# Kernel tuning notes

Hardware: AMD Instinct MI355X
Metric: run time of the kernel (lower is better)

Reference implementation:

```python
import jax, jax.numpy as jnp
import numpy as np

B, L, D = 2, 2048, 1024
N_HEADS, N_KV_HEADS = 16, 4
HEAD_DIM = D // N_HEADS
WINDOW = 1024
ROPE_BASE = 10000.0


def setup_inputs() -> dict:
    key = jax.random.key(0)
    ks = jax.random.split(key, 5)
    s = 0.02
    return {
        "x": jax.random.normal(ks[0], (B, L, D), jnp.float32),
        "Wq": jax.random.normal(ks[1], (D, N_HEADS * HEAD_DIM), jnp.float32) * s,
        "Wk": jax.random.normal(ks[2], (D, N_KV_HEADS * HEAD_DIM), jnp.float32) * s,
        "Wv": jax.random.normal(ks[3], (D, N_KV_HEADS * HEAD_DIM), jnp.float32) * s,
        "Wo": jax.random.normal(ks[4], (N_HEADS * HEAD_DIM, D), jnp.float32) * s,
    }


def _rope_cos_sin(seq_len, head_dim, dtype):
    inv_freq = 1.0 / (ROPE_BASE ** (jnp.arange(0, head_dim, 2, dtype=jnp.float32) / head_dim))
    angles = jnp.arange(seq_len, dtype=jnp.float32)[:, None] * inv_freq[None, :]  # [L, d/2]
    emb = jnp.concatenate([angles, angles], axis=-1)  # [L, d]
    return jnp.cos(emb).astype(dtype), jnp.sin(emb).astype(dtype)


def _rotate_half(t):
    t1, t2 = jnp.split(t, 2, axis=-1)
    return jnp.concatenate([-t2, t1], axis=-1)


def reference(x, Wq, Wk, Wv, Wo):
    b, l, d = x.shape
    q = (x @ Wq).reshape(b, l, N_HEADS, HEAD_DIM).transpose(0, 2, 1, 3)      # [B,H,L,d]
    k = (x @ Wk).reshape(b, l, N_KV_HEADS, HEAD_DIM).transpose(0, 2, 1, 3)   # [B,Kv,L,d]
    v = (x @ Wv).reshape(b, l, N_KV_HEADS, HEAD_DIM).transpose(0, 2, 1, 3)

    cos, sin = _rope_cos_sin(l, HEAD_DIM, x.dtype)  # [L,d]
    q = q * cos[None, None] + _rotate_half(q) * sin[None, None]
    k = k * cos[None, None] + _rotate_half(k) * sin[None, None]

    # GQA: expand kv heads to query heads
    group = N_HEADS // N_KV_HEADS
    k = jnp.repeat(k, group, axis=1)  # [B,H,L,d]
    v = jnp.repeat(v, group, axis=1)

    scale = 1.0 / np.sqrt(HEAD_DIM)
    scores = jnp.einsum("bhqd,bhkd->bhqk", q, k) * scale  # [B,H,L,L]

    # sliding-window causal mask: attend to j with j <= i and i - j < WINDOW
    i = jnp.arange(l)[:, None]
    j = jnp.arange(l)[None, :]
    allowed = (j <= i) & (i - j < WINDOW)
    scores = jnp.where(allowed[None, None], scores, jnp.finfo(scores.dtype).min)

    attn = jax.nn.softmax(scores, axis=-1)
    out = jnp.einsum("bhqk,bhkd->bhqd", attn, v)           # [B,H,L,d]
    out = out.transpose(0, 2, 1, 3).reshape(b, l, N_HEADS * HEAD_DIM)
    return out @ Wo  # [B,L,D]; dropout p=0 is identity
```

## Files before the change

kernel.cpp:

```cpp
#include <hip/hip_runtime.h>

typedef unsigned short u16;
typedef unsigned int u32;
typedef short short8 __attribute__((ext_vector_type(8)));
typedef float f32x4 __attribute__((ext_vector_type(4)));

#define N_B 2
#define N_L 2048
#define N_D 1024
#define N_H 16
#define N_KVH 4
#define HDIM 64
#define WINDOW 1024

#define QSCALE (0.125f * 1.44269504088896f)

__device__ __forceinline__ u16 f2bf(float f) {
  unsigned u = __builtin_bit_cast(unsigned, f);
  u = u + 0x7fffu + ((u >> 16) & 1u);
  return (u16)(u >> 16);
}

__device__ __forceinline__ u32 pk2bf(float lo, float hi) {
  u32 a = __builtin_bit_cast(u32, lo) + 0x8000u;
  u32 b = __builtin_bit_cast(u32, hi) + 0x8000u;
  return __builtin_amdgcn_perm(b, a, 0x07060302u);
}

__device__ __forceinline__ void gl2lds16(const u16* g, u16* l) {
  __builtin_amdgcn_global_load_lds((const __attribute__((address_space(1))) void*)g,
                                   (__attribute__((address_space(3))) void*)l, 16, 0, 0);
}


__global__ __launch_bounds__(256) void prep_kernel(
    const float* __restrict__ x, const float* __restrict__ Wq, const float* __restrict__ Wk,
    const float* __restrict__ Wv, const float* __restrict__ Wo,
    u16* __restrict__ xb, u16* __restrict__ wqkvT, u16* __restrict__ woT,
    float* __restrict__ rc, float* __restrict__ rs) {
  __shared__ float tbuf[32][33];
  int bid = blockIdx.x, tid = threadIdx.x;
  if (bid < 1024) {
    size_t base = ((size_t)bid * 256 + tid) * 16;
    u32 o[8];
#pragma unroll
    for (int j = 0; j < 4; j++) {
      float4 f = *(const float4*)&x[base + j * 4];
      o[2 * j] = pk2bf(f.x, f.y);
      o[2 * j + 1] = pk2bf(f.z, f.w);
    }
    *(uint4*)&xb[base] = *(uint4*)&o[0];
    *(uint4*)&xb[base + 8] = *(uint4*)&o[4];
  } else if (bid < 3584) {
    const float* src;
    u16* dst;
    int gx, t, shift;
    if (bid < 2048) { src = Wq; dst = wqkvT; gx = 32; shift = 5; t = bid - 1024; }
    else if (bid < 2304) { src = Wk; dst = wqkvT + 1024 * 1024; gx = 8; shift = 3; t = bid - 2048; }
    else if (bid < 2560) { src = Wv; dst = wqkvT + 1280 * 1024; gx = 8; shift = 3; t = bid - 2304; }
    else { src = Wo; dst = woT; gx = 32; shift = 5; t = bid - 2560; }
    int srcN = gx * 32;
    int n0 = (t & (gx - 1)) * 32, k0 = (t >> shift) * 32;
    int lx = tid & 31, ly = tid >> 5;
#pragma unroll
    for (int q = 0; q < 4; q++)
      tbuf[ly + 8 * q][lx] = src[(k0 + ly + 8 * q) * srcN + n0 + lx];
    __syncthreads();
#pragma unroll
    for (int q = 0; q < 4; q++)
      dst[(n0 + ly + 8 * q) * 1024 + k0 + lx] = f2bf(tbuf[lx][ly + 8 * q]);
  } else {
    int idx = (bid - 3584) * 256 + tid;
    int i = idx >> 5, j = idx & 31;
    float inv = powf(10000.0f, -(float)j * (1.0f / 32.0f));
    float ang = (float)i * inv;
    rc[idx] = cosf(ang);
    rs[idx] = sinf(ang);
  }
}


template <int MODE>
__global__ __launch_bounds__(256, 2) void gemm_kernel(
    const u16* __restrict__ A, const u16* __restrict__ Bt,
    u16* __restrict__ qo, u16* __restrict__ ko, u16* __restrict__ vo,
    float* __restrict__ fo, const float* __restrict__ rc, const float* __restrict__ rs) {
  __shared__ u16 smem[65536 / 2];
  int tid = threadIdx.x;
  int w = tid >> 6, lane = tid & 63, quad = lane >> 4, r = lane & 15;
  int rx = r & 7;
  int wm = w >> 1, wn = w & 1;
  int m0 = blockIdx.y * 128, n0 = blockIdx.x * 128;

  f32x4 acc[4][4];
#pragma unroll
  for (int a_ = 0; a_ < 4; a_++)
#pragma unroll
    for (int b_ = 0; b_ < 4; b_++) acc[a_][b_] = {0.f, 0.f, 0.f, 0.f};

  auto stage = [&](int kt, int buf) {
    u16* a_s = smem + buf * 8192;
    u16* b_s = smem + 16384 + buf * 8192;
#pragma unroll
    for (int it = 0; it < 4; ++it) {
      int cc = it * 256 + tid;
      int row = cc >> 3, p = cc & 7, c = p ^ (row & 7);
      gl2lds16(&A[(size_t)(m0 + row) * 1024 + kt * 64 + c * 8], &a_s[cc * 8]);
    }
#pragma unroll
    for (int it = 0; it < 4; ++it) {
      int cc = it * 256 + tid;
      int row = cc >> 3, p = cc & 7, c = p ^ (row & 7);
      gl2lds16(&Bt[(size_t)(n0 + row) * 1024 + kt * 64 + c * 8], &b_s[cc * 8]);
    }
  };

  stage(0, 0);
  for (int kt = 0; kt < 16; ++kt) {
    int buf = kt & 1;
    __syncthreads();
    if (kt + 1 < 16) stage(kt + 1, buf ^ 1);
    u16* a_s = smem + buf * 8192;
    u16* b_s = smem + 16384 + buf * 8192;
#pragma unroll
    for (int ks = 0; ks < 2; ks++) {
      int pc = (ks * 4 + quad) ^ rx;
      short8 af[4], bfr[4];
#pragma unroll
      for (int tm = 0; tm < 4; tm++)
        af[tm] = *(const short8*)&a_s[(wm * 64 + tm * 16 + r) * 64 + pc * 8];
#pragma unroll
      for (int tn = 0; tn < 4; tn++)
        bfr[tn] = *(const short8*)&b_s[(wn * 64 + tn * 16 + r) * 64 + pc * 8];
#pragma unroll
      for (int tm = 0; tm < 4; tm++)
#pragma unroll
        for (int tn = 0; tn < 4; tn++)
          acc[tm][tn] = __builtin_amdgcn_mfma_f32_16x16x32_bf16(af[tm], bfr[tn], acc[tm][tn], 0, 0, 0);
    }
  }

  int nbase = n0 + wn * 64;
  if constexpr (MODE == 0) {
    if (nbase < 1024) {
      int h = nbase >> 6;
#pragma unroll
      for (int tm = 0; tm < 4; tm++) {
#pragma unroll
        for (int reg = 0; reg < 4; reg++) {
          int m = m0 + wm * 64 + tm * 16 + quad * 4 + reg;
          int b = m >> 11, i = m & 2047;
          size_t base = ((size_t)(b * N_H + h) * N_L + i) * HDIM;
#pragma unroll
          for (int tn = 0; tn < 2; tn++) {
            int dlo = tn * 16 + r;
            float c = rc[i * 32 + dlo], s = rs[i * 32 + dlo];
            float vlo = acc[tm][tn][reg], vhi = acc[tm][tn + 2][reg];
            qo[base + dlo] = f2bf((vlo * c - vhi * s) * QSCALE);
            qo[base + dlo + 32] = f2bf((vhi * c + vlo * s) * QSCALE);
          }
        }
      }
    } else if (nbase < 1280) {
      int h = (nbase - 1024) >> 6;
#pragma unroll
      for (int tm = 0; tm < 4; tm++) {
#pragma unroll
        for (int reg = 0; reg < 4; reg++) {
          int m = m0 + wm * 64 + tm * 16 + quad * 4 + reg;
          int b = m >> 11, i = m & 2047;
          size_t base = ((size_t)(b * N_KVH + h) * N_L + i) * HDIM;
#pragma unroll
          for (int tn = 0; tn < 2; tn++) {
            int dlo = tn * 16 + r;
            float c = rc[i * 32 + dlo], s = rs[i * 32 + dlo];
            float vlo = acc[tm][tn][reg], vhi = acc[tm][tn + 2][reg];
            ko[base + dlo] = f2bf(vlo * c - vhi * s);
            ko[base + dlo + 32] = f2bf(vhi * c + vlo * s);
          }
        }
      }
    } else {
      __syncthreads();
      int hkv = (nbase - 1280) >> 6;
      int bb = (m0 + wm * 64) >> 11;
      int tbase = (m0 + wm * 64) & 2047;
      u16* myvs = smem + w * 4608;
#pragma unroll
      for (int tm = 0; tm < 4; tm++) {
#pragma unroll
        for (int tn = 0; tn < 4; tn++) {
          uint2 pk;
          pk.x = pk2bf(acc[tm][tn][0], acc[tm][tn][1]);
          pk.y = pk2bf(acc[tm][tn][2], acc[tm][tn][3]);
          *(uint2*)&myvs[(tn * 16 + r) * 72 + tm * 16 + quad * 4] = pk;
        }
      }
      __asm__ volatile("s_waitcnt lgkmcnt(0)" ::: "memory");
      u16* vtb = vo + (size_t)((bb * N_KVH + hkv) * 64) * 2048;
#pragma unroll
      for (int q2 = 0; q2 < 8; ++q2) {
        int flat = q2 * 64 + lane;
        int row = flat >> 3, part = flat & 7;
        uint4 val = *(uint4*)&myvs[row * 72 + part * 8];
        *(uint4*)&vtb[row * 2048 + tbase + part * 8] = val;
      }
    }
  } else {
#pragma unroll
    for (int tm = 0; tm < 4; tm++) {
#pragma unroll
      for (int reg = 0; reg < 4; reg++) {
        int m = m0 + wm * 64 + tm * 16 + quad * 4 + reg;
#pragma unroll
        for (int tn = 0; tn < 4; tn++)
          fo[(size_t)m * 1024 + nbase + tn * 16 + r] = acc[tm][tn][reg];
      }
    }
  }
}


__global__ __launch_bounds__(256) void attn_kernel(
    const u16* __restrict__ Q, const u16* __restrict__ K,
    const u16* __restrict__ Vt, u16* __restrict__ O) {
  __shared__ u16 k_s[2][64 * 64];
  __shared__ u16 v_s[2][64 * 64];
  __shared__ u16 pt[4][16 * 64];
  int tid = threadIdx.x, w = tid >> 6, lane = tid & 63, quad = lane >> 4, r = lane & 15;
  int qb = 31 - blockIdx.x;
  int h = blockIdx.y, b = blockIdx.z;
  int i0 = qb * 64;
  int hk = h >> 2;
  int qw0 = i0 + w * 16;
  int iq = qw0 + r;

  const u16* qptr = Q + (size_t)((b * N_H + h) * N_L + iq) * HDIM;
  short8 qf[2];
  qf[0] = *(const short8*)&qptr[quad * 8];
  qf[1] = *(const short8*)&qptr[32 + quad * 8];

  const u16* kbase = K + (size_t)(b * N_KVH + hk) * N_L * HDIM;
  const u16* vtbase = Vt + (size_t)(b * N_KVH + hk) * HDIM * N_L;

  auto stage = [&](int jt, int buf) {
#pragma unroll
    for (int it = 0; it < 2; ++it) {
      int cc = it * 256 + tid;
      int row = cc >> 3, p = cc & 7, c = p ^ (row & 7);
      gl2lds16(&kbase[(size_t)(jt * 64 + row) * 64 + c * 8], &k_s[buf][cc * 8]);
    }
#pragma unroll
    for (int it = 0; it < 2; ++it) {
      int cc = it * 256 + tid;
      int row = cc >> 3, p = cc & 7, c = p ^ (row & 7);
      gl2lds16(&vtbase[(size_t)row * 2048 + jt * 64 + c * 8], &v_s[buf][cc * 8]);
    }
  };

  float l_lane = 0.f;
  f32x4 o_acc[4];
#pragma unroll
  for (int tm = 0; tm < 4; tm++) o_acc[tm] = {0.f, 0.f, 0.f, 0.f};

  int jt0 = (i0 >= WINDOW) ? ((i0 - (WINDOW - 1)) >> 6) : 0;
  int nt = qb - jt0 + 1;
  u16* mypt = pt[w];
  int rx = r & 7;

  stage(jt0, 0);

  for (int t = 0; t < nt; ++t) {
    int jt = jt0 + t, j0 = jt << 6, buf = t & 1;
    __syncthreads();
    if (t + 1 < nt) stage(jt + 1, buf ^ 1);

    f32x4 s_acc[4];
#pragma unroll
    for (int tm = 0; tm < 4; tm++) s_acc[tm] = {0.f, 0.f, 0.f, 0.f};
#pragma unroll
    for (int ks = 0; ks < 2; ks++) {
      int pc = (ks * 4 + quad) ^ rx;
#pragma unroll
      for (int tm = 0; tm < 4; tm++) {
        short8 kf = *(const short8*)&k_s[buf][(tm * 16 + r) * 64 + pc * 8];
        s_acc[tm] = __builtin_amdgcn_mfma_f32_16x16x32_bf16(kf, qf[ks], s_acc[tm], 0, 0, 0);
      }
    }

    bool interior = (j0 + 63 <= qw0) && (qw0 + 15 - j0 < WINDOW);
    if (!interior) {
#pragma unroll
      for (int tm = 0; tm < 4; tm++) {
#pragma unroll
        for (int reg = 0; reg < 4; reg++) {
          int j = j0 + tm * 16 + quad * 4 + reg;
          bool ok = (j <= iq) && (iq - j < WINDOW);
          if (!ok) s_acc[tm][reg] = -1e30f;
        }
      }
    }

    float p[4][4];
#pragma unroll
    for (int tm = 0; tm < 4; tm++)
#pragma unroll
      for (int reg = 0; reg < 4; reg++) {
        float e = __builtin_amdgcn_exp2f(s_acc[tm][reg]);
        p[tm][reg] = e;
        l_lane += e;
      }

#pragma unroll
    for (int tm = 0; tm < 4; tm++) {
      uint2 pk;
      pk.x = pk2bf(p[tm][0], p[tm][1]);
      pk.y = pk2bf(p[tm][2], p[tm][3]);
      int c = tm * 2 + (quad >> 1), half = quad & 1;
      int pp = c ^ rx;
      *(uint2*)&mypt[r * 64 + pp * 8 + half * 4] = pk;
    }
    __asm__ volatile("s_waitcnt lgkmcnt(0)" ::: "memory");

#pragma unroll
    for (int ks = 0; ks < 2; ks++) {
      int pc = (ks * 4 + quad) ^ rx;
      short8 bp = *(const short8*)&mypt[r * 64 + pc * 8];
#pragma unroll
      for (int tm = 0; tm < 4; tm++) {
        short8 av = *(const short8*)&v_s[buf][(tm * 16 + r) * 64 + pc * 8];
        o_acc[tm] = __builtin_amdgcn_mfma_f32_16x16x32_bf16(av, bp, o_acc[tm], 0, 0, 0);
      }
    }
  }

  l_lane += __shfl_xor(l_lane, 16);
  l_lane += __shfl_xor(l_lane, 32);
  float inv = 1.0f / l_lane;
  size_t obase = (size_t)(b * N_L + iq) * 1024 + h * 64;
#pragma unroll
  for (int tm = 0; tm < 4; tm++) {
    uint2 pk;
    pk.x = pk2bf(o_acc[tm][0] * inv, o_acc[tm][1] * inv);
    pk.y = pk2bf(o_acc[tm][2] * inv, o_acc[tm][3] * inv);
    *(uint2*)&O[obase + tm * 16 + quad * 4] = pk;
  }
}


extern "C" void kernel_launch(void* const* d_in, const int* in_sizes, int n_in,
                              void* d_out, int out_size, void* d_ws, size_t ws_size,
                              hipStream_t stream) {
  const float* x = (const float*)d_in[0];
  const float* Wq = (const float*)d_in[1];
  const float* Wk = (const float*)d_in[2];
  const float* Wv = (const float*)d_in[3];
  const float* Wo = (const float*)d_in[4];
  float* out = (float*)d_out;
  char* ws = (char*)d_ws;

  u16* xb    = (u16*)(ws);
  u16* wqkvT = (u16*)(ws + 0x800000);
  u16* woT   = (u16*)(ws + 0xB00000);
  u16* Qb    = (u16*)(ws + 0xD00000);
  u16* Kb    = (u16*)(ws + 0x1500000);
  u16* Vtb   = (u16*)(ws + 0x1700000);
  u16* Ob    = (u16*)(ws + 0x1900000);
  float* rc  = (float*)(ws + 0x2100000);
  float* rs  = (float*)(ws + 0x2140000);

  prep_kernel<<<3840, 256, 0, stream>>>(x, Wq, Wk, Wv, Wo, xb, wqkvT, woT, rc, rs);
  gemm_kernel<0><<<dim3(12, 32), 256, 0, stream>>>(xb, wqkvT, Qb, Kb, Vtb, nullptr, rc, rs);
  attn_kernel<<<dim3(32, 16, 2), 256, 0, stream>>>(Qb, Kb, Vtb, Ob);
  gemm_kernel<1><<<dim3(8, 32), 256, 0, stream>>>(Ob, woT, nullptr, nullptr, nullptr, out, nullptr, nullptr);
}
```

Measured before the change: 147.9 us.

## Process two 64-row query subtiles per attention block to reuse K/V tiles

```diff
diff --git a/kernel.cpp b/kernel.cpp
--- a/kernel.cpp
+++ b/kernel.cpp
@@ -228,17 +228,19 @@
   __shared__ u16 v_s[2][64 * 64];
   __shared__ u16 pt[4][16 * 64];
   int tid = threadIdx.x, w = tid >> 6, lane = tid & 63, quad = lane >> 4, r = lane & 15;
-  int qb = 31 - blockIdx.x;
+  int qp = 15 - blockIdx.x;
   int h = blockIdx.y, b = blockIdx.z;
-  int i0 = qb * 64;
+  int i0 = qp * 128;
   int hk = h >> 2;
-  int qw0 = i0 + w * 16;
-  int iq = qw0 + r;
-
-  const u16* qptr = Q + (size_t)((b * N_H + h) * N_L + iq) * HDIM;
-  short8 qf[2];
-  qf[0] = *(const short8*)&qptr[quad * 8];
-  qf[1] = *(const short8*)&qptr[32 + quad * 8];
+  int rx = r & 7;
+
+  short8 qf[2][2];
+#pragma unroll
+  for (int s = 0; s < 2; s++) {
+    const u16* qptr = Q + (size_t)((b * N_H + h) * N_L + i0 + s * 64 + w * 16 + r) * HDIM;
+    qf[s][0] = *(const short8*)&qptr[quad * 8];
+    qf[s][1] = *(const short8*)&qptr[32 + quad * 8];
+  }
 
   const u16* kbase = K + (size_t)(b * N_KVH + hk) * N_L * HDIM;
   const u16* vtbase = Vt + (size_t)(b * N_KVH + hk) * HDIM * N_L;
@@ -258,15 +260,16 @@
     }
   };
 
-  float l_lane = 0.f;
-  f32x4 o_acc[4];
-#pragma unroll
-  for (int tm = 0; tm < 4; tm++) o_acc[tm] = {0.f, 0.f, 0.f, 0.f};
+  float l_lane[2] = {0.f, 0.f};
+  f32x4 o_acc[2][4];
+#pragma unroll
+  for (int s = 0; s < 2; s++)
+#pragma unroll
+    for (int tm = 0; tm < 4; tm++) o_acc[s][tm] = {0.f, 0.f, 0.f, 0.f};
 
   int jt0 = (i0 >= WINDOW) ? ((i0 - (WINDOW - 1)) >> 6) : 0;
-  int nt = qb - jt0 + 1;
+  int nt = (2 * qp + 1) - jt0 + 1;
   u16* mypt = pt[w];
-  int rx = r & 7;
 
   stage(jt0, 0);
 
@@ -275,75 +278,91 @@
     __syncthreads();
     if (t + 1 < nt) stage(jt + 1, buf ^ 1);
 
-    f32x4 s_acc[4];
-#pragma unroll
-    for (int tm = 0; tm < 4; tm++) s_acc[tm] = {0.f, 0.f, 0.f, 0.f};
+    short8 kf[2][4];
 #pragma unroll
     for (int ks = 0; ks < 2; ks++) {
       int pc = (ks * 4 + quad) ^ rx;
 #pragma unroll
+      for (int tm = 0; tm < 4; tm++)
+        kf[ks][tm] = *(const short8*)&k_s[buf][(tm * 16 + r) * 64 + pc * 8];
+    }
+
+#pragma unroll
+    for (int s = 0; s < 2; s++) {
+      int qw0 = i0 + s * 64 + w * 16;
+      int iq = qw0 + r;
+
+      f32x4 s_acc[4];
+#pragma unroll
+      for (int tm = 0; tm < 4; tm++) s_acc[tm] = {0.f, 0.f, 0.f, 0.f};
+#pragma unroll
+      for (int ks = 0; ks < 2; ks++)
+#pragma unroll
+        for (int tm = 0; tm < 4; tm++)
+          s_acc[tm] = __builtin_amdgcn_mfma_f32_16x16x32_bf16(kf[ks][tm], qf[s][ks], s_acc[tm], 0, 0, 0);
+
+      bool interior = (j0 + 63 <= qw0) && (qw0 + 15 - j0 < WINDOW);
+      if (!interior) {
+#pragma unroll
+        for (int tm = 0; tm < 4; tm++) {
+#pragma unroll
+          for (int reg = 0; reg < 4; reg++) {
+            int j = j0 + tm * 16 + quad * 4 + reg;
+            bool ok = (j <= iq) && (iq - j < WINDOW);
+            if (!ok) s_acc[tm][reg] = -1e30f;
+          }
+        }
+      }
+
+      float p[4][4];
+#pragma unroll
+      for (int tm = 0; tm < 4; tm++)
+#pragma unroll
+        for (int reg = 0; reg < 4; reg++) {
+          float e = __builtin_amdgcn_exp2f(s_acc[tm][reg]);
+          p[tm][reg] = e;
+          l_lane[s] += e;
+        }
+
+#pragma unroll
       for (int tm = 0; tm < 4; tm++) {
-        short8 kf = *(const short8*)&k_s[buf][(tm * 16 + r) * 64 + pc * 8];
-        s_acc[tm] = __builtin_amdgcn_mfma_f32_16x16x32_bf16(kf, qf[ks], s_acc[tm], 0, 0, 0);
-      }
-    }
-
-    bool interior = (j0 + 63 <= qw0) && (qw0 + 15 - j0 < WINDOW);
-    if (!interior) {
-#pragma unroll
-      for (int tm = 0; tm < 4; tm++) {
-#pragma unroll
-        for (int reg = 0; reg < 4; reg++) {
-          int j = j0 + tm * 16 + quad * 4 + reg;
-          bool ok = (j <= iq) && (iq - j < WINDOW);
-          if (!ok) s_acc[tm][reg] = -1e30f;
-        }
-      }
-    }
-
-    float p[4][4];
-#pragma unroll
-    for (int tm = 0; tm < 4; tm++)
-#pragma unroll
-      for (int reg = 0; reg < 4; reg++) {
-        float e = __builtin_amdgcn_exp2f(s_acc[tm][reg]);
-        p[tm][reg] = e;
-        l_lane += e;
-      }
-
+        uint2 pk;
+        pk.x = pk2bf(p[tm][0], p[tm][1]);
+        pk.y = pk2bf(p[tm][2], p[tm][3]);
+        int c = tm * 2 + (quad >> 1), half = quad & 1;
+        int pp = c ^ rx;
+        *(uint2*)&mypt[r * 64 + pp * 8 + half * 4] = pk;
+      }
+      __asm__ volatile("s_waitcnt lgkmcnt(0)" ::: "memory");
+
+#pragma unroll
+      for (int ks = 0; ks < 2; ks++) {
+        int pc = (ks * 4 + quad) ^ rx;
+        short8 bp = *(const short8*)&mypt[r * 64 + pc * 8];
+#pragma unroll
+        for (int tm = 0; tm < 4; tm++) {
+          short8 av = *(const short8*)&v_s[buf][(tm * 16 + r) * 64 + pc * 8];
+          o_acc[s][tm] = __builtin_amdgcn_mfma_f32_16x16x32_bf16(av, bp, o_acc[s][tm], 0, 0, 0);
+        }
+      }
+    }
+  }
+
+#pragma unroll
+  for (int s = 0; s < 2; s++) {
+    float l = l_lane[s];
+    l += __shfl_xor(l, 16);
+    l += __shfl_xor(l, 32);
+    float inv = 1.0f / l;
+    int iq = i0 + s * 64 + w * 16 + r;
+    size_t obase = (size_t)(b * N_L + iq) * 1024 + h * 64;
 #pragma unroll
     for (int tm = 0; tm < 4; tm++) {
       uint2 pk;
-      pk.x = pk2bf(p[tm][0], p[tm][1]);
-      pk.y = pk2bf(p[tm][2], p[tm][3]);
-      int c = tm * 2 + (quad >> 1), half = quad & 1;
-      int pp = c ^ rx;
-      *(uint2*)&mypt[r * 64 + pp * 8 + half * 4] = pk;
-    }
-    __asm__ volatile("s_waitcnt lgkmcnt(0)" ::: "memory");
-
-#pragma unroll
-    for (int ks = 0; ks < 2; ks++) {
-      int pc = (ks * 4 + quad) ^ rx;
-      short8 bp = *(const short8*)&mypt[r * 64 + pc * 8];
-#pragma unroll
-      for (int tm = 0; tm < 4; tm++) {
-        short8 av = *(const short8*)&v_s[buf][(tm * 16 + r) * 64 + pc * 8];
-        o_acc[tm] = __builtin_amdgcn_mfma_f32_16x16x32_bf16(av, bp, o_acc[tm], 0, 0, 0);
-      }
-    }
-  }
-
-  l_lane += __shfl_xor(l_lane, 16);
-  l_lane += __shfl_xor(l_lane, 32);
-  float inv = 1.0f / l_lane;
-  size_t obase = (size_t)(b * N_L + iq) * 1024 + h * 64;
-#pragma unroll
-  for (int tm = 0; tm < 4; tm++) {
-    uint2 pk;
-    pk.x = pk2bf(o_acc[tm][0] * inv, o_acc[tm][1] * inv);
-    pk.y = pk2bf(o_acc[tm][2] * inv, o_acc[tm][3] * inv);
-    *(uint2*)&O[obase + tm * 16 + quad * 4] = pk;
+      pk.x = pk2bf(o_acc[s][tm][0] * inv, o_acc[s][tm][1] * inv);
+      pk.y = pk2bf(o_acc[s][tm][2] * inv, o_acc[s][tm][3] * inv);
+      *(uint2*)&O[obase + tm * 16 + quad * 4] = pk;
+    }
   }
 }
 
@@ -371,6 +390,6 @@
 
   prep_kernel<<<3840, 256, 0, stream>>>(x, Wq, Wk, Wv, Wo, xb, wqkvT, woT, rc, rs);
   gemm_kernel<0><<<dim3(12, 32), 256, 0, stream>>>(xb, wqkvT, Qb, Kb, Vtb, nullptr, rc, rs);
-  attn_kernel<<<dim3(32, 16, 2), 256, 0, stream>>>(Qb, Kb, Vtb, Ob);
+  attn_kernel<<<dim3(16, 16, 2), 256, 0, stream>>>(Qb, Kb, Vtb, Ob);
   gemm_kernel<1><<<dim3(8, 32), 256, 0, stream>>>(Ob, woT, nullptr, nullptr, nullptr, out, nullptr, nullptr);
 }
```

Result: slower. 154.9 us (+4.8%).
